# Performance work log

Hardware: AMD Instinct MI355X
Metric: run time of the kernel (lower is better)

## Reference

```python
import jax, jax.numpy as jnp
import numpy as np

LEAKY_ALPHA = 0.2  # tf.nn.leaky_relu default
L2_EPS = 1e-12     # tf.nn.l2_normalize default epsilon


def setup_inputs() -> dict:
    key = jax.random.key(0)
    ks = jax.random.split(key, 6)
    N, E, D, K = 100000, 1280000, 64, 3
    x = jax.random.normal(ks[0], (N, D), dtype=jnp.float32)
    edge_index = jax.random.randint(ks[1], (2, E), 0, N, dtype=jnp.int64)
    W1 = jax.random.normal(ks[2], (K, D, D), dtype=jnp.float32) * 0.1
    b1 = jnp.zeros((K, D), dtype=jnp.float32)
    W2 = jax.random.normal(ks[3], (K, D, D), dtype=jnp.float32) * 0.1
    b2 = jnp.zeros((K, D), dtype=jnp.float32)
    return {"x": x, "edge_index": edge_index, "W1": W1, "b1": b1, "W2": W2, "b2": b2}


def _leaky(z):
    return jnp.where(z > 0, z, LEAKY_ALPHA * z)


def _l2_normalize(h):
    sq = jnp.sum(h * h, axis=-1, keepdims=True)
    return h * jax.lax.rsqrt(jnp.maximum(sq, L2_EPS))


def reference(x, edge_index, W1, b1, W2, b2):
    N = x.shape[0]
    K = W1.shape[0]
    row, col = edge_index[0], edge_index[1]
    # LightGCN-style symmetric normalization: D^-1/2 A D^-1/2
    deg = jax.ops.segment_sum(jnp.ones_like(row, dtype=x.dtype), row, num_segments=N)
    dinv = jnp.where(deg > 0, jax.lax.rsqrt(jnp.maximum(deg, 1.0)), 0.0)
    norm = dinv[row] * dinv[col]  # [E]

    h = x
    h_list = [h]
    for i in range(K):
        # sparse SpMM: agg = normed_adj @ h
        msg = h[col] * norm[:, None]                       # [E, D] gather + scale
        agg = jax.ops.segment_sum(msg, row, num_segments=N)  # [N, D] scatter-add
        # dual dense transform + elementwise gate
        h = _leaky(agg @ W1[i] + b1[i]) + _leaky((h * agg) @ W2[i] + b2[i])
        h_list.append(_l2_normalize(h))
    return jnp.concatenate(h_list, axis=-1)  # [N, D + K*units]
```

## Files before the change

### kernel.cpp

```cpp
#include <hip/hip_runtime.h>

#define LEAKY 0.2f
#define SCAN_BS 256

typedef __attribute__((ext_vector_type(8))) short bf16x8;
typedef __attribute__((ext_vector_type(4))) float f32x4;

__device__ __forceinline__ unsigned short f2bf(float f) {
    unsigned u = __float_as_uint(f);
    u += 0x7FFF + ((u >> 16) & 1);
    return (unsigned short)(u >> 16);
}
__device__ __forceinline__ float bf2f(unsigned short u) {
    return __uint_as_float((unsigned)u << 16);
}

__global__ __launch_bounds__(256) void zero_kernel(int4* __restrict__ p, int n4) {
    int i = blockIdx.x * 256 + threadIdx.x;
    if (i < n4) p[i] = (int4){0, 0, 0, 0};
}

__global__ __launch_bounds__(256) void hist_rank_kernel(const int* __restrict__ row, int E,
                                                        int* __restrict__ deg,
                                                        int* __restrict__ rank) {
    int base = (blockIdx.x * 256 + threadIdx.x) * 4;
    if (base + 4 <= E) {
        int4 r = *reinterpret_cast<const int4*>(row + base);
        int4 k;
        k.x = atomicAdd(&deg[r.x], 1);
        k.y = atomicAdd(&deg[r.y], 1);
        k.z = atomicAdd(&deg[r.z], 1);
        k.w = atomicAdd(&deg[r.w], 1);
        *reinterpret_cast<int4*>(rank + base) = k;
    } else {
        for (int e = base; e < E; ++e) rank[e] = atomicAdd(&deg[row[e]], 1);
    }
}

__global__ __launch_bounds__(SCAN_BS) void bsum_kernel(const int* __restrict__ deg,
                                                       int* __restrict__ bsums, int n) {
    int i = blockIdx.x * SCAN_BS + threadIdx.x;
    int v = (i < n) ? deg[i] : 0;
    for (int off = 32; off; off >>= 1) v += __shfl_xor(v, off, 64);
    __shared__ int wsum[SCAN_BS / 64];
    int lane = threadIdx.x & 63, w = threadIdx.x >> 6;
    if (lane == 0) wsum[w] = v;
    __syncthreads();
    if (threadIdx.x == 0) {
        int s = 0;
#pragma unroll
        for (int j = 0; j < SCAN_BS / 64; ++j) s += wsum[j];
        bsums[blockIdx.x] = s;
    }
}

__global__ __launch_bounds__(1024) void scan_bsums_kernel(int* __restrict__ bsums, int nb) {
    __shared__ int sh[1024];
    int tid = threadIdx.x;
    int v = (tid < nb) ? bsums[tid] : 0;
    sh[tid] = v;
    __syncthreads();
    for (int off = 1; off < 1024; off <<= 1) {
        int u = (tid >= off) ? sh[tid - off] : 0;
        __syncthreads();
        sh[tid] += u;
        __syncthreads();
    }
    if (tid < nb) bsums[tid] = sh[tid] - v;
}

__global__ __launch_bounds__(SCAN_BS) void rowptr_dinv_kernel(const int* __restrict__ deg,
                                                              const int* __restrict__ bsums_ex,
                                                              int* __restrict__ rowptr,
                                                              float* __restrict__ dinv, int n) {
    __shared__ int sh[SCAN_BS];
    int tid = threadIdx.x;
    int i = blockIdx.x * SCAN_BS + tid;
    int v = (i < n) ? deg[i] : 0;
    sh[tid] = v;
    __syncthreads();
    for (int off = 1; off < SCAN_BS; off <<= 1) {
        int u = (tid >= off) ? sh[tid - off] : 0;
        __syncthreads();
        sh[tid] += u;
        __syncthreads();
    }
    if (i <= n) rowptr[i] = sh[tid] - v + bsums_ex[blockIdx.x];
    if (i < n) dinv[i] = v > 0 ? rsqrtf((float)v) : 0.0f;
}

__global__ __launch_bounds__(256) void scatter_store_kernel(const int* __restrict__ row,
                                                            const int* __restrict__ col,
                                                            const int* __restrict__ rank, int E,
                                                            const int* __restrict__ rowptr,
                                                            int* __restrict__ cols_s) {
    int base = (blockIdx.x * 256 + threadIdx.x) * 4;
    if (base + 4 <= E) {
        int4 r = *reinterpret_cast<const int4*>(row + base);
        int4 c = *reinterpret_cast<const int4*>(col + base);
        int4 k = *reinterpret_cast<const int4*>(rank + base);
        int p0 = rowptr[r.x];
        int p1 = rowptr[r.y];
        int p2 = rowptr[r.z];
        int p3 = rowptr[r.w];
        cols_s[p0 + k.x] = c.x;
        cols_s[p1 + k.y] = c.y;
        cols_s[p2 + k.z] = c.z;
        cols_s[p3 + k.w] = c.w;
    } else {
        for (int e = base; e < E; ++e) cols_s[rowptr[row[e]] + rank[e]] = col[e];
    }
}

__global__ __launch_bounds__(256) void scale_kernel(const float* __restrict__ dinv,
                                                    const float* __restrict__ len,
                                                    float* __restrict__ scale, int n) {
    int i = blockIdx.x * 256 + threadIdx.x;
    if (i < n) scale[i] = dinv[i] * len[i];
}

__global__ __launch_bounds__(256) void aggregate_kernel(const int* __restrict__ rowptr,
                                                        const int* __restrict__ cols_s,
                                                        const float* __restrict__ scale,
                                                        const float* __restrict__ dinv,
                                                        const unsigned short* __restrict__ h_bf,
                                                        unsigned short* __restrict__ agg_bf,
                                                        int n_nodes) {
    int lane = threadIdx.x & 63;
    int n = (blockIdx.x * blockDim.x + threadIdx.x) >> 6;
    if (n >= n_nodes) return;
    int nu = __builtin_amdgcn_readfirstlane(n);
    int s = rowptr[nu];
    int e = rowptr[nu + 1];
    int eg = lane >> 3;
    int dsl = lane & 7;

    float accA[8] = {0, 0, 0, 0, 0, 0, 0, 0};
    float accB[8] = {0, 0, 0, 0, 0, 0, 0, 0};
    for (int t = s; t < e; t += 16) {
        int i0 = t + eg;
        int i1 = t + 8 + eg;
        bool v0 = i0 < e;
        bool v1 = i1 < e;
        int c0 = cols_s[v0 ? i0 : (e - 1)];
        int c1 = cols_s[v1 ? i1 : (e - 1)];
        float w0 = v0 ? scale[c0] : 0.0f;
        float w1 = v1 ? scale[c1] : 0.0f;
        bf16x8 h0 = *reinterpret_cast<const bf16x8*>(h_bf + ((size_t)c0 << 6) + dsl * 8);
        bf16x8 h1 = *reinterpret_cast<const bf16x8*>(h_bf + ((size_t)c1 << 6) + dsl * 8);
#pragma unroll
        for (int j = 0; j < 8; ++j) accA[j] = fmaf(w0, bf2f((unsigned short)h0[j]), accA[j]);
#pragma unroll
        for (int j = 0; j < 8; ++j) accB[j] = fmaf(w1, bf2f((unsigned short)h1[j]), accB[j]);
    }
    float dn = dinv[nu];
#pragma unroll
    for (int j = 0; j < 8; ++j) {
        float a = accA[j] + accB[j];
        a += __shfl_xor(a, 8, 64);
        a += __shfl_xor(a, 16, 64);
        a += __shfl_xor(a, 32, 64);
        accA[j] = a * dn;
    }
    if (lane < 8) {
        bf16x8 o;
#pragma unroll
        for (int j = 0; j < 8; ++j) o[j] = (short)f2bf(accA[j]);
        *reinterpret_cast<bf16x8*>(agg_bf + ((size_t)nu << 6) + lane * 8) = o;
    }
}

__global__ __launch_bounds__(256, 3) void transform_kernel(const unsigned short* __restrict__ h_bf,
                                                           const float* __restrict__ len_in,
                                                           const unsigned short* __restrict__ agg_bf,
                                                           const float* __restrict__ w1,
                                                           const float* __restrict__ b1,
                                                           const float* __restrict__ w2,
                                                           const float* __restrict__ b2,
                                                           float* __restrict__ out_norm,
                                                           int ostride,
                                                           float* __restrict__ len_out,
                                                           unsigned short* __restrict__ hbf_out,
                                                           int n_nodes) {
    int lane = threadIdx.x & 63;
    int wave = (blockIdx.x * blockDim.x + threadIdx.x) >> 6;
    int n0 = wave * 16;
    if (n0 >= n_nodes) return;

    int r16 = lane & 15;
    int g   = lane >> 4;

    bf16x8 w1f[2][4], w2f[2][4];
#pragma unroll
    for (int kt = 0; kt < 2; ++kt) {
#pragma unroll
        for (int dt = 0; dt < 4; ++dt) {
            const float* p1 = w1 + (kt * 32 + 8 * g) * 64 + dt * 16 + r16;
            const float* p2 = w2 + (kt * 32 + 8 * g) * 64 + dt * 16 + r16;
            bf16x8 f1, f2;
#pragma unroll
            for (int j = 0; j < 8; ++j) {
                f1[j] = (short)f2bf(p1[(size_t)j * 64]);
                f2[j] = (short)f2bf(p2[(size_t)j * 64]);
            }
            w1f[kt][dt] = f1;
            w2f[kt][dt] = f2;
        }
    }

    int row = n0 + r16;
    if (row >= n_nodes) row = n_nodes - 1;
    float lv = len_in ? len_in[row] : 1.0f;

    f32x4 acc1[4], acc2[4];
#pragma unroll
    for (int dt = 0; dt < 4; ++dt) {
        acc1[dt] = (f32x4){0.0f, 0.0f, 0.0f, 0.0f};
        acc2[dt] = (f32x4){0.0f, 0.0f, 0.0f, 0.0f};
    }

#pragma unroll
    for (int kt = 0; kt < 2; ++kt) {
        const unsigned short* ap = agg_bf + ((size_t)row << 6) + kt * 32 + 8 * g;
        const unsigned short* hp = h_bf + ((size_t)row << 6) + kt * 32 + 8 * g;
        bf16x8 af = *reinterpret_cast<const bf16x8*>(ap);
        bf16x8 h8 = *reinterpret_cast<const bf16x8*>(hp);
        bf16x8 mf;
#pragma unroll
        for (int j = 0; j < 8; ++j) {
            mf[j] = (short)f2bf(bf2f((unsigned short)af[j]) * bf2f((unsigned short)h8[j]) * lv);
        }
#pragma unroll
        for (int dt = 0; dt < 4; ++dt) {
            acc1[dt] = __builtin_amdgcn_mfma_f32_16x16x32_bf16(af, w1f[kt][dt], acc1[dt], 0, 0, 0);
            acc2[dt] = __builtin_amdgcn_mfma_f32_16x16x32_bf16(mf, w2f[kt][dt], acc2[dt], 0, 0, 0);
        }
    }

    float b1v[4], b2v[4];
#pragma unroll
    for (int dt = 0; dt < 4; ++dt) {
        b1v[dt] = b1[dt * 16 + r16];
        b2v[dt] = b2[dt * 16 + r16];
    }
    float v[4][4];
#pragma unroll
    for (int dt = 0; dt < 4; ++dt) {
#pragma unroll
        for (int reg = 0; reg < 4; ++reg) {
            float x1 = acc1[dt][reg] + b1v[dt];
            float x2 = acc2[dt][reg] + b2v[dt];
            x1 = x1 > 0.0f ? x1 : LEAKY * x1;
            x2 = x2 > 0.0f ? x2 : LEAKY * x2;
            v[dt][reg] = x1 + x2;
        }
    }
#pragma unroll
    for (int reg = 0; reg < 4; ++reg) {
        float sq = v[0][reg] * v[0][reg] + v[1][reg] * v[1][reg] +
                   v[2][reg] * v[2][reg] + v[3][reg] * v[3][reg];
        sq += __shfl_xor(sq, 1, 64);
        sq += __shfl_xor(sq, 2, 64);
        sq += __shfl_xor(sq, 4, 64);
        sq += __shfl_xor(sq, 8, 64);
        float m = fmaxf(sq, 1e-12f);
        float inv = rsqrtf(m);
        int orow = n0 + 4 * g + reg;
        if (orow < n_nodes) {
#pragma unroll
            for (int dt = 0; dt < 4; ++dt) {
                float nv = v[dt][reg] * inv;
                out_norm[(size_t)orow * ostride + dt * 16 + r16] = nv;
                hbf_out[((size_t)orow << 6) + dt * 16 + r16] = f2bf(nv);
            }
            if (r16 == reg) len_out[orow] = sqrtf(m);
        }
    }
}

__global__ __launch_bounds__(256) void copyx_kernel(const float* __restrict__ x,
                                                    float* __restrict__ out,
                                                    unsigned short* __restrict__ x_bf,
                                                    int n_nodes, int nslots) {
    int t = blockIdx.x * 256 + threadIdx.x;
    int total = n_nodes * 16;
    if (t >= total) return;
    int node = t >> 4;
    int j = t & 15;
    float4 v = reinterpret_cast<const float4*>(x)[(size_t)node * 16 + j];
    reinterpret_cast<float4*>(out)[(size_t)node * (nslots * 16) + j] = v;
    ushort4 b;
    b.x = f2bf(v.x); b.y = f2bf(v.y); b.z = f2bf(v.z); b.w = f2bf(v.w);
    reinterpret_cast<ushort4*>(x_bf)[(size_t)node * 16 + j] = b;
}

extern "C" void kernel_launch(void* const* d_in, const int* in_sizes, int n_in,
                              void* d_out, int out_size, void* d_ws, size_t ws_size,
                              hipStream_t stream) {
    const float* x  = (const float*)d_in[0];
    const int*  edge = (const int*)d_in[1];
    const float* W1 = (const float*)d_in[2];
    const float* b1 = (const float*)d_in[3];
    const float* W2 = (const float*)d_in[4];
    const float* b2 = (const float*)d_in[5];

    const int N = in_sizes[0] / 64;
    const int E = in_sizes[1] / 2;
    const int K = in_sizes[2] / 4096;
    const int nslots = K + 1;
    const int ostride = nslots * 64;

    const int* row = edge;
    const int* col = edge + E;
    float* out = (float*)d_out;

    char* ws = (char*)d_ws;
    size_t off = 0;
    auto carve = [&](size_t bytes) -> void* {
        void* p = ws + off;
        off = (off + bytes + 255) & ~(size_t)255;
        return p;
    };
    int*   deg     = (int*)  carve((size_t)N * 4);
    int*   rowptr  = (int*)  carve((size_t)(N + 1) * 4);
    float* dinv    = (float*)carve((size_t)N * 4);
    float* scale   = (float*)carve((size_t)N * 4);
    float* len     = (float*)carve((size_t)N * 4);
    int*   rank    = (int*)  carve((size_t)E * 4);
    int*   cols_s  = (int*)  carve((size_t)E * 4);
    unsigned short* agg_bf = (unsigned short*)carve((size_t)N * 64 * 2);
    unsigned short* hbfA = (unsigned short*)carve((size_t)N * 64 * 2);
    unsigned short* hbfB = (unsigned short*)carve((size_t)N * 64 * 2);
    int*   bsums   = (int*)  carve(2048 * 4);
    (void)ws_size;

    const int n4 = (N + 3) / 4;
    zero_kernel<<<(n4 + 255) / 256, 256, 0, stream>>>((int4*)deg, n4);

    const int eblk4 = (E + 256 * 4 - 1) / (256 * 4);
    hist_rank_kernel<<<eblk4, 256, 0, stream>>>(row, E, deg, rank);

    const int nb = (N + 1 + SCAN_BS - 1) / SCAN_BS;
    bsum_kernel<<<nb, SCAN_BS, 0, stream>>>(deg, bsums, N);
    scan_bsums_kernel<<<1, 1024, 0, stream>>>(bsums, nb);
    rowptr_dinv_kernel<<<nb, SCAN_BS, 0, stream>>>(deg, bsums, rowptr, dinv, N);

    scatter_store_kernel<<<eblk4, 256, 0, stream>>>(row, col, rank, E, rowptr, cols_s);

    copyx_kernel<<<(N * 16 + 255) / 256, 256, 0, stream>>>(x, out, hbfA, N, nslots);

    const int waves_needed = (N + 15) / 16;
    const int tblocks = (waves_needed + 3) / 4;
    const int nblk256 = (N + 255) / 256;

    unsigned short* hin = hbfA;
    unsigned short* hout = hbfB;
    for (int i = 0; i < K; ++i) {
        const float* len_in;
        const float* sc;
        if (i == 0) {
            len_in = nullptr; sc = dinv;
        } else {
            len_in = len;
            scale_kernel<<<nblk256, 256, 0, stream>>>(dinv, len, scale, N);
            sc = scale;
        }
        aggregate_kernel<<<(N * 64 + 255) / 256, 256, 0, stream>>>(rowptr, cols_s, sc, dinv,
                                                                   hin, agg_bf, N);
        transform_kernel<<<tblocks, 256, 0, stream>>>(hin, len_in, agg_bf,
                                                      W1 + (size_t)i * 4096,
                                                      b1 + (size_t)i * 64,
                                                      W2 + (size_t)i * 4096,
                                                      b2 + (size_t)i * 64,
                                                      out + (size_t)(i + 1) * 64,
                                                      ostride, len, hout, N);
        unsigned short* tmp = hin; hin = hout; hout = tmp;
    }
}
```

Baseline: 273.8 us.

## Prepack bf16 weight fragments, fuse scale and zero kernels, use nontemporal output stores

Adds a one-time kernel that converts W1/W2 into per-lane bf16 MFMA fragment layout, so each transform wave loads packed 16-byte vectors instead of doing strided fp32 loads and conversions. The per-node scale (dinv*len) is now written by the transform kernel, which removes the separate scale kernel, and the degree zeroing is folded into the copy-x kernel. Output stores become nontemporal. Together these cut launch count and per-wave weight-preparation work, at the cost of an extra small workspace buffer and one extra prep launch.

```diff
diff --git a/kernel.cpp b/kernel.cpp
--- a/kernel.cpp
+++ b/kernel.cpp
@@ -15,9 +15,24 @@
     return __uint_as_float((unsigned)u << 16);
 }
 
-__global__ __launch_bounds__(256) void zero_kernel(int4* __restrict__ p, int n4) {
-    int i = blockIdx.x * 256 + threadIdx.x;
-    if (i < n4) p[i] = (int4){0, 0, 0, 0};
+__global__ __launch_bounds__(256) void wprep_kernel(const float* __restrict__ w1,
+                                                    const float* __restrict__ w2,
+                                                    unsigned short* __restrict__ wfrag,
+                                                    int total) {
+    int t = blockIdx.x * 256 + threadIdx.x;
+    if (t >= total) return;
+    int lane = t & 63;
+    int dt = (t >> 6) & 3;
+    int kt = (t >> 8) & 1;
+    int m  = (t >> 9) & 1;
+    int L  = t >> 10;
+    int r16 = lane & 15, g = lane >> 4;
+    const float* wsrc = (m == 0 ? w1 : w2) + (size_t)L * 4096;
+    const float* p = wsrc + (kt * 32 + 8 * g) * 64 + dt * 16 + r16;
+    bf16x8 f;
+#pragma unroll
+    for (int j = 0; j < 8; ++j) f[j] = (short)f2bf(p[(size_t)j * 64]);
+    *reinterpret_cast<bf16x8*>(wfrag + (size_t)t * 8) = f;
 }
 
 __global__ __launch_bounds__(256) void hist_rank_kernel(const int* __restrict__ row, int E,
@@ -112,13 +127,6 @@
     }
 }
 
-__global__ __launch_bounds__(256) void scale_kernel(const float* __restrict__ dinv,
-                                                    const float* __restrict__ len,
-                                                    float* __restrict__ scale, int n) {
-    int i = blockIdx.x * 256 + threadIdx.x;
-    if (i < n) scale[i] = dinv[i] * len[i];
-}
-
 __global__ __launch_bounds__(256) void aggregate_kernel(const int* __restrict__ rowptr,
                                                         const int* __restrict__ cols_s,
                                                         const float* __restrict__ scale,
@@ -173,13 +181,14 @@
 __global__ __launch_bounds__(256, 3) void transform_kernel(const unsigned short* __restrict__ h_bf,
                                                            const float* __restrict__ len_in,
                                                            const unsigned short* __restrict__ agg_bf,
-                                                           const float* __restrict__ w1,
+                                                           const unsigned short* __restrict__ wfrag,
                                                            const float* __restrict__ b1,
-                                                           const float* __restrict__ w2,
                                                            const float* __restrict__ b2,
+                                                           const float* __restrict__ dinv,
                                                            float* __restrict__ out_norm,
                                                            int ostride,
                                                            float* __restrict__ len_out,
+                                                           float* __restrict__ scale_out,
                                                            unsigned short* __restrict__ hbf_out,
                                                            int n_nodes) {
     int lane = threadIdx.x & 63;
@@ -195,16 +204,10 @@
     for (int kt = 0; kt < 2; ++kt) {
 #pragma unroll
         for (int dt = 0; dt < 4; ++dt) {
-            const float* p1 = w1 + (kt * 32 + 8 * g) * 64 + dt * 16 + r16;
-            const float* p2 = w2 + (kt * 32 + 8 * g) * 64 + dt * 16 + r16;
-            bf16x8 f1, f2;
-#pragma unroll
-            for (int j = 0; j < 8; ++j) {
-                f1[j] = (short)f2bf(p1[(size_t)j * 64]);
-                f2[j] = (short)f2bf(p2[(size_t)j * 64]);
-            }
-            w1f[kt][dt] = f1;
-            w2f[kt][dt] = f2;
+            w1f[kt][dt] = *reinterpret_cast<const bf16x8*>(
+                wfrag + (((size_t)(0 * 2 + kt) * 4 + dt) * 64 + lane) * 8);
+            w2f[kt][dt] = *reinterpret_cast<const bf16x8*>(
+                wfrag + (((size_t)(1 * 2 + kt) * 4 + dt) * 64 + lane) * 8);
         }
     }
 
@@ -270,25 +273,31 @@
 #pragma unroll
             for (int dt = 0; dt < 4; ++dt) {
                 float nv = v[dt][reg] * inv;
-                out_norm[(size_t)orow * ostride + dt * 16 + r16] = nv;
+                __builtin_nontemporal_store(nv, &out_norm[(size_t)orow * ostride + dt * 16 + r16]);
                 hbf_out[((size_t)orow << 6) + dt * 16 + r16] = f2bf(nv);
             }
-            if (r16 == reg) len_out[orow] = sqrtf(m);
-        }
-    }
-}
-
-__global__ __launch_bounds__(256) void copyx_kernel(const float* __restrict__ x,
-                                                    float* __restrict__ out,
-                                                    unsigned short* __restrict__ x_bf,
-                                                    int n_nodes, int nslots) {
+            if (r16 == reg) {
+                float ln = sqrtf(m);
+                len_out[orow] = ln;
+                scale_out[orow] = dinv[orow] * ln;
+            }
+        }
+    }
+}
+
+__global__ __launch_bounds__(256) void copyx_zero_kernel(const float* __restrict__ x,
+                                                         float* __restrict__ out,
+                                                         unsigned short* __restrict__ x_bf,
+                                                         int4* __restrict__ deg4, int n4,
+                                                         int n_nodes, int nslots) {
     int t = blockIdx.x * 256 + threadIdx.x;
+    if (t < n4) deg4[t] = (int4){0, 0, 0, 0};
     int total = n_nodes * 16;
     if (t >= total) return;
     int node = t >> 4;
     int j = t & 15;
-    float4 v = reinterpret_cast<const float4*>(x)[(size_t)node * 16 + j];
-    reinterpret_cast<float4*>(out)[(size_t)node * (nslots * 16) + j] = v;
+    f32x4 v = reinterpret_cast<const f32x4*>(x)[(size_t)node * 16 + j];
+    __builtin_nontemporal_store(v, &reinterpret_cast<f32x4*>(out)[(size_t)node * (nslots * 16) + j]);
     ushort4 b;
     b.x = f2bf(v.x); b.y = f2bf(v.y); b.z = f2bf(v.z); b.w = f2bf(v.w);
     reinterpret_cast<ushort4*>(x_bf)[(size_t)node * 16 + j] = b;
@@ -321,7 +330,8 @@
         off = (off + bytes + 255) & ~(size_t)255;
         return p;
     };
-    int*   deg     = (int*)  carve((size_t)N * 4);
+    const int n4 = (N + 3) / 4;
+    int*   deg     = (int*)  carve((size_t)n4 * 16);
     int*   rowptr  = (int*)  carve((size_t)(N + 1) * 4);
     float* dinv    = (float*)carve((size_t)N * 4);
     float* scale   = (float*)carve((size_t)N * 4);
@@ -331,11 +341,15 @@
     unsigned short* agg_bf = (unsigned short*)carve((size_t)N * 64 * 2);
     unsigned short* hbfA = (unsigned short*)carve((size_t)N * 64 * 2);
     unsigned short* hbfB = (unsigned short*)carve((size_t)N * 64 * 2);
+    unsigned short* wfrag = (unsigned short*)carve((size_t)K * 2 * 2 * 4 * 64 * 8 * 2);
     int*   bsums   = (int*)  carve(2048 * 4);
     (void)ws_size;
 
-    const int n4 = (N + 3) / 4;
-    zero_kernel<<<(n4 + 255) / 256, 256, 0, stream>>>((int4*)deg, n4);
+    copyx_zero_kernel<<<(N * 16 + 255) / 256, 256, 0, stream>>>(x, out, hbfA,
+                                                                (int4*)deg, n4, N, nslots);
+
+    const int wtotal = K * 2 * 2 * 4 * 64;
+    wprep_kernel<<<(wtotal + 255) / 256, 256, 0, stream>>>(W1, W2, wfrag, wtotal);
 
     const int eblk4 = (E + 256 * 4 - 1) / (256 * 4);
     hist_rank_kernel<<<eblk4, 256, 0, stream>>>(row, E, deg, rank);
@@ -347,33 +361,23 @@
 
     scatter_store_kernel<<<eblk4, 256, 0, stream>>>(row, col, rank, E, rowptr, cols_s);
 
-    copyx_kernel<<<(N * 16 + 255) / 256, 256, 0, stream>>>(x, out, hbfA, N, nslots);
-
     const int waves_needed = (N + 15) / 16;
     const int tblocks = (waves_needed + 3) / 4;
-    const int nblk256 = (N + 255) / 256;
 
     unsigned short* hin = hbfA;
     unsigned short* hout = hbfB;
     for (int i = 0; i < K; ++i) {
-        const float* len_in;
-        const float* sc;
-        if (i == 0) {
-            len_in = nullptr; sc = dinv;
-        } else {
-            len_in = len;
-            scale_kernel<<<nblk256, 256, 0, stream>>>(dinv, len, scale, N);
-            sc = scale;
-        }
+        const float* len_in = (i == 0) ? nullptr : len;
+        const float* sc = (i == 0) ? dinv : scale;
         aggregate_kernel<<<(N * 64 + 255) / 256, 256, 0, stream>>>(rowptr, cols_s, sc, dinv,
                                                                    hin, agg_bf, N);
         transform_kernel<<<tblocks, 256, 0, stream>>>(hin, len_in, agg_bf,
-                                                      W1 + (size_t)i * 4096,
+                                                      wfrag + (size_t)i * 2 * 2 * 4 * 64 * 8,
                                                       b1 + (size_t)i * 64,
-                                                      W2 + (size_t)i * 4096,
                                                       b2 + (size_t)i * 64,
+                                                      dinv,
                                                       out + (size_t)(i + 1) * 64,
-                                                      ostride, len, hout, N);
+                                                      ostride, len, scale, hout, N);
         unsigned short* tmp = hin; hin = hout; hout = tmp;
     }
 }
```

After: 257.6 us. 1.06x faster.
